# Kernel tuning notes

Measured on AMD Instinct MI355X. Metric: run time of the kernel, lower is better.

Reference implementation:

```python
import jax, jax.numpy as jnp
import numpy as np

N_NODES = 100000
N_EDGES = 800000
IN_SIZE = 256
OUT_SIZE = 256


def setup_inputs() -> dict:
    key = jax.random.key(0)
    k1, k2, k3, k4, k5, k6 = jax.random.split(key, 6)
    stdv = 1.0 / np.sqrt(OUT_SIZE)
    x = jax.random.normal(k1, (N_NODES, IN_SIZE), dtype=jnp.float32)
    weight = jax.random.uniform(k2, (IN_SIZE, OUT_SIZE), dtype=jnp.float32, minval=-stdv, maxval=stdv)
    bias = jax.random.uniform(k3, (1, OUT_SIZE), dtype=jnp.float32, minval=-stdv, maxval=stdv)
    edge_weight = jax.random.uniform(k4, (N_EDGES,), dtype=jnp.float32)
    edge_src = jax.random.randint(k5, (N_EDGES,), 0, N_NODES, dtype=jnp.int32)
    edge_dst = jax.random.randint(k6, (N_EDGES,), 0, N_NODES, dtype=jnp.int32)
    return {"x": x, "weight": weight, "bias": bias,
            "edge_weight": edge_weight, "edge_src": edge_src, "edge_dst": edge_dst}


def reference(x, weight, bias, edge_weight, edge_src, edge_dst):
    # supp = input @ W  (dense GEMM)
    supp = jnp.matmul(x, weight)  # [N, out]
    # out = spmm(A, supp): A in COO form -> gather source rows, scale, scatter-add to dst
    msgs = supp[edge_src] * edge_weight[:, None]  # [E, out]
    agg = jax.ops.segment_sum(msgs, edge_dst, num_segments=x.shape[0])  # [N, out]
    return agg + bias
```

## Files before the change

### kernel.cpp

```cpp
#include <hip/hip_runtime.h>
#include <hip/hip_bf16.h>

#define N_NODES 100000
#define N_EDGES 800000
#define K_DIM 256
#define N_DIM 256

typedef __attribute__((ext_vector_type(8)))  short  bf16x8;
typedef __attribute__((ext_vector_type(4)))  short  bf16x4;
typedef __attribute__((ext_vector_type(4)))  float  f32x4;

__device__ short g_Wt[K_DIM * N_DIM];
__device__ int   g_bsums[512];
__device__ int   g_boff[512];

static __device__ inline short f32_to_bf16s(float f) {
    __bf16 h = (__bf16)f;
    return __builtin_bit_cast(short, h);
}
static __device__ inline float bf16s_to_f32(short s) {
    unsigned int u = ((unsigned int)(unsigned short)s) << 16;
    return __uint_as_float(u);
}

__global__ __launch_bounds__(256) void convert_w_kernel(const float* __restrict__ W) {
    const int n = blockIdx.x;
    const int k = threadIdx.x;
    g_Wt[n * K_DIM + k] = f32_to_bf16s(W[(size_t)k * N_DIM + n]);
}

__global__ __launch_bounds__(256) void mfma_gemm_kernel(const float* __restrict__ X,
                                                        short* __restrict__ Sb,
                                                        int M) {
    const int wave = threadIdx.x >> 6;
    const int lane = threadIdx.x & 63;
    const int r    = lane & 15;
    const int kg   = lane >> 4;
    const int m0   = blockIdx.x * 64;
    const int wc   = wave * 64;

    f32x4 acc[4][4];
    #pragma unroll
    for (int i = 0; i < 4; ++i)
        #pragma unroll
        for (int j = 0; j < 4; ++j)
            acc[i][j] = (f32x4)0.f;

    #pragma unroll
    for (int k0 = 0; k0 < K_DIM; k0 += 32) {
        bf16x8 a[4], b[4];
        #pragma unroll
        for (int mi = 0; mi < 4; ++mi) {
            int row = m0 + mi * 16 + r;
            row = row < M ? row : (M - 1);
            const float* p = X + (size_t)row * K_DIM + k0 + kg * 8;
            f32x4 lo = *reinterpret_cast<const f32x4*>(p);
            f32x4 hi = *reinterpret_cast<const f32x4*>(p + 4);
            bf16x8 v;
            v[0] = f32_to_bf16s(lo[0]); v[1] = f32_to_bf16s(lo[1]);
            v[2] = f32_to_bf16s(lo[2]); v[3] = f32_to_bf16s(lo[3]);
            v[4] = f32_to_bf16s(hi[0]); v[5] = f32_to_bf16s(hi[1]);
            v[6] = f32_to_bf16s(hi[2]); v[7] = f32_to_bf16s(hi[3]);
            a[mi] = v;
        }
        #pragma unroll
        for (int ni = 0; ni < 4; ++ni) {
            const short* q = g_Wt + (size_t)(wc + ni * 16 + r) * K_DIM + k0 + kg * 8;
            b[ni] = *reinterpret_cast<const bf16x8*>(q);
        }
        #pragma unroll
        for (int mi = 0; mi < 4; ++mi)
            #pragma unroll
            for (int ni = 0; ni < 4; ++ni)
                acc[mi][ni] = __builtin_amdgcn_mfma_f32_16x16x32_bf16(a[mi], b[ni], acc[mi][ni], 0, 0, 0);
    }

    #pragma unroll
    for (int mi = 0; mi < 4; ++mi) {
        #pragma unroll
        for (int reg = 0; reg < 4; ++reg) {
            const int row = m0 + mi * 16 + kg * 4 + reg;
            if (row < M) {
                #pragma unroll
                for (int ni = 0; ni < 4; ++ni)
                    Sb[(size_t)row * N_DIM + wc + ni * 16 + r] = f32_to_bf16s(acc[mi][ni][reg]);
            }
        }
    }
}

__global__ __launch_bounds__(256) void count_kernel(const int* __restrict__ edst,
                                                    int* __restrict__ counts, int E) {
    int e = blockIdx.x * 256 + threadIdx.x;
    if (e < E) atomicAdd(&counts[edst[e]], 1);
}

#define SCAN_NB ((N_NODES + 255) / 256)

__global__ __launch_bounds__(256) void scan1_kernel(const int* __restrict__ counts) {
    __shared__ int wsum[4];
    const int i = blockIdx.x * 256 + threadIdx.x;
    int v = (i < N_NODES) ? counts[i] : 0;
    #pragma unroll
    for (int st = 32; st > 0; st >>= 1) v += __shfl_down(v, st, 64);
    if ((threadIdx.x & 63) == 0) wsum[threadIdx.x >> 6] = v;
    __syncthreads();
    if (threadIdx.x == 0) g_bsums[blockIdx.x] = wsum[0] + wsum[1] + wsum[2] + wsum[3];
}

__global__ __launch_bounds__(512) void scan2_kernel() {
    __shared__ int s[512];
    const int t = threadIdx.x;
    int v = (t < SCAN_NB) ? g_bsums[t] : 0;
    s[t] = v;
    __syncthreads();
    for (int st = 1; st < 512; st <<= 1) {
        int u = (t >= st) ? s[t - st] : 0;
        __syncthreads();
        s[t] += u;
        __syncthreads();
    }
    g_boff[t] = s[t] - v;
}

__global__ __launch_bounds__(256) void scan3_kernel(const int* __restrict__ counts,
                                                    int* __restrict__ offsets,
                                                    int* __restrict__ cursor) {
    __shared__ int s[256];
    const int t = threadIdx.x;
    const int i = blockIdx.x * 256 + t;
    int v = (i < N_NODES) ? counts[i] : 0;
    s[t] = v;
    __syncthreads();
    for (int st = 1; st < 256; st <<= 1) {
        int u = (t >= st) ? s[t - st] : 0;
        __syncthreads();
        s[t] += u;
        __syncthreads();
    }
    if (i < N_NODES) {
        int inc = g_boff[blockIdx.x] + s[t];
        offsets[i + 1] = inc;
        cursor[i]      = inc - v;
    }
    if (i == 0) offsets[0] = 0;
}

__global__ __launch_bounds__(256) void fill_kernel(const int* __restrict__ esrc,
                                                   const int* __restrict__ edst,
                                                   const float* __restrict__ ew,
                                                   int* __restrict__ cursor,
                                                   int2* __restrict__ csr, int E) {
    int e = blockIdx.x * 256 + threadIdx.x;
    if (e >= E) return;
    int pos = atomicAdd(&cursor[edst[e]], 1);
    csr[pos] = make_int2(esrc[e], __float_as_int(ew[e]));
}

__global__ __launch_bounds__(256) void gather_kernel(const short* __restrict__ Sb,
                                                     const float* __restrict__ bias,
                                                     const int* __restrict__ offsets,
                                                     const int2* __restrict__ csr,
                                                     float* __restrict__ out) {
    const int tid  = threadIdx.x;
    const int node = blockIdx.x * 4 + (tid >> 6);
    if (node >= N_NODES) return;
    const int lane = tid & 63;

    const int row = offsets[node];
    const int end = offsets[node + 1];

    f32x4 acc = *reinterpret_cast<const f32x4*>(bias + lane * 4);

    int j = row;
    for (; j + 2 <= end; j += 2) {
        const int2 p0 = csr[j];
        const int2 p1 = csr[j + 1];
        const bf16x4 v0 = *reinterpret_cast<const bf16x4*>(Sb + (size_t)p0.x * N_DIM + lane * 4);
        const bf16x4 v1 = *reinterpret_cast<const bf16x4*>(Sb + (size_t)p1.x * N_DIM + lane * 4);
        const float w0 = __int_as_float(p0.y);
        const float w1 = __int_as_float(p1.y);
        #pragma unroll
        for (int c = 0; c < 4; ++c)
            acc[c] += bf16s_to_f32(v0[c]) * w0 + bf16s_to_f32(v1[c]) * w1;
    }
    if (j < end) {
        const int2 p = csr[j];
        const bf16x4 v = *reinterpret_cast<const bf16x4*>(Sb + (size_t)p.x * N_DIM + lane * 4);
        const float w = __int_as_float(p.y);
        #pragma unroll
        for (int c = 0; c < 4; ++c)
            acc[c] += bf16s_to_f32(v[c]) * w;
    }

    *reinterpret_cast<f32x4*>(out + (size_t)node * N_DIM + lane * 4) = acc;
}

__global__ __launch_bounds__(256) void init_out_kernel(float* __restrict__ out,
                                                       const float* __restrict__ bias,
                                                       int total) {
    int i = blockIdx.x * 256 + threadIdx.x;
    if (i < total) out[i] = bias[i & (N_DIM - 1)];
}

__global__ __launch_bounds__(256) void scatter_kernel(const short* __restrict__ Sb,
                                                      const float* __restrict__ ew,
                                                      const int* __restrict__ esrc,
                                                      const int* __restrict__ edst,
                                                      float* __restrict__ out, int E) {
    const int tid  = threadIdx.x;
    const int e    = blockIdx.x * 4 + (tid >> 6);
    if (e >= E) return;
    const int lane = tid & 63;
    const int   s = esrc[e];
    const int   d = edst[e];
    const float w = ew[e];
    const bf16x4 v = *reinterpret_cast<const bf16x4*>(Sb + (size_t)s * N_DIM + lane * 4);
    float* o = out + (size_t)d * N_DIM + lane * 4;
    unsafeAtomicAdd(o + 0, bf16s_to_f32(v[0]) * w);
    unsafeAtomicAdd(o + 1, bf16s_to_f32(v[1]) * w);
    unsafeAtomicAdd(o + 2, bf16s_to_f32(v[2]) * w);
    unsafeAtomicAdd(o + 3, bf16s_to_f32(v[3]) * w);
}

extern "C" void kernel_launch(void* const* d_in, const int* in_sizes, int n_in,
                              void* d_out, int out_size, void* d_ws, size_t ws_size,
                              hipStream_t stream) {
    const float* x      = (const float*)d_in[0];
    const float* weight = (const float*)d_in[1];
    const float* bias   = (const float*)d_in[2];
    const float* ew     = (const float*)d_in[3];
    const int*   esrc   = (const int*)d_in[4];
    const int*   edst   = (const int*)d_in[5];
    float*       out    = (float*)d_out;

    char*  ws     = (char*)d_ws;
    const size_t SUPP_B = ((size_t)N_NODES * N_DIM * 2 + 255) & ~(size_t)255;
    const size_t CNT_B  = (size_t)N_NODES * 4;
    const size_t OFF_B  = ((size_t)(N_NODES + 1) * 4 + 15) & ~(size_t)15;
    const size_t CSR_B  = (size_t)N_EDGES * 8;

    short* supp    = (short*)(ws);
    int*   counts  = (int*)  (ws + SUPP_B);
    int*   cursor  = (int*)  (ws + SUPP_B + CNT_B);
    int*   offsets = (int*)  (ws + SUPP_B + 2 * CNT_B);
    int2*  csr     = (int2*) (ws + SUPP_B + 2 * CNT_B + OFF_B);
    const size_t NEEDED = SUPP_B + 2 * CNT_B + OFF_B + CSR_B;

    convert_w_kernel<<<N_DIM, 256, 0, stream>>>(weight);
    mfma_gemm_kernel<<<(N_NODES + 63) / 64, 256, 0, stream>>>(x, supp, N_NODES);

    if (ws_size >= NEEDED) {
        (void)hipMemsetAsync(counts, 0, CNT_B, stream);
        count_kernel<<<(N_EDGES + 255) / 256, 256, 0, stream>>>(edst, counts, N_EDGES);
        scan1_kernel<<<SCAN_NB, 256, 0, stream>>>(counts);
        scan2_kernel<<<1, 512, 0, stream>>>();
        scan3_kernel<<<SCAN_NB, 256, 0, stream>>>(counts, offsets, cursor);
        fill_kernel<<<(N_EDGES + 255) / 256, 256, 0, stream>>>(esrc, edst, ew,
                                                               cursor, csr, N_EDGES);
        gather_kernel<<<(N_NODES + 3) / 4, 256, 0, stream>>>(supp, bias, offsets, csr, out);
    } else {
        int total = N_NODES * N_DIM;
        init_out_kernel<<<(total + 255) / 256, 256, 0, stream>>>(out, bias, total);
        scatter_kernel<<<(N_EDGES + 3) / 4, 256, 0, stream>>>(supp, ew, esrc, edst, out, N_EDGES);
    }
}
```

Measured before the change: 414.1 us.

## Stage GEMM A tiles in LDS with double-buffered async global_load_lds

The fp32 X tile for each 64-row block is now loaded once per block into a double-buffered, XOR-swizzled LDS buffer using global_load_lds. Previously all four waves fetched the same A rows from global memory on their own. The load of the next K-slice overlaps with the current slice's MFMA work. The cost is extra LDS use and a barrier per K step, and correctness depends on the async LDS loads having completed before each barrier.

```diff
diff --git a/kernel.cpp b/kernel.cpp
--- a/kernel.cpp
+++ b/kernel.cpp
@@ -29,14 +29,20 @@
     g_Wt[n * K_DIM + k] = f32_to_bf16s(W[(size_t)k * N_DIM + n]);
 }
 
+#define GBM 64
+#define GBK 32
+
 __global__ __launch_bounds__(256) void mfma_gemm_kernel(const float* __restrict__ X,
                                                         short* __restrict__ Sb,
                                                         int M) {
-    const int wave = threadIdx.x >> 6;
-    const int lane = threadIdx.x & 63;
+    __shared__ float A_lds[2][GBM * GBK];
+
+    const int tid  = threadIdx.x;
+    const int wave = tid >> 6;
+    const int lane = tid & 63;
     const int r    = lane & 15;
     const int kg   = lane >> 4;
-    const int m0   = blockIdx.x * 64;
+    const int m0   = blockIdx.x * GBM;
     const int wc   = wave * 64;
 
     f32x4 acc[4][4];
@@ -46,16 +52,39 @@
         for (int j = 0; j < 4; ++j)
             acc[i][j] = (f32x4)0.f;
 
-    #pragma unroll
-    for (int k0 = 0; k0 < K_DIM; k0 += 32) {
-        bf16x8 a[4], b[4];
+    auto stage = [&](int buf, int k0) {
+        #pragma unroll
+        for (int p = 0; p < 2; ++p) {
+            const int d   = p * 256 + tid;
+            const int row = d >> 3;
+            const int cc  = (d & 7) ^ (row & 7);
+            int gr = m0 + row;
+            gr = gr < M ? gr : (M - 1);
+            const float* gp = X + (size_t)gr * K_DIM + k0 + cc * 4;
+            float* lp = &A_lds[buf][d * 4];
+            __builtin_amdgcn_global_load_lds(
+                (const __attribute__((address_space(1))) void*)gp,
+                (__attribute__((address_space(3))) void*)lp, 16, 0, 0);
+        }
+    };
+
+    stage(0, 0);
+    __syncthreads();
+
+    for (int t = 0; t < K_DIM / GBK; ++t) {
+        const int cur = t & 1;
+        if (t + 1 < K_DIM / GBK) stage(cur ^ 1, (t + 1) * GBK);
+
+        const int k0 = t * GBK;
+
+        bf16x8 a[4];
         #pragma unroll
         for (int mi = 0; mi < 4; ++mi) {
-            int row = m0 + mi * 16 + r;
-            row = row < M ? row : (M - 1);
-            const float* p = X + (size_t)row * K_DIM + k0 + kg * 8;
-            f32x4 lo = *reinterpret_cast<const f32x4*>(p);
-            f32x4 hi = *reinterpret_cast<const f32x4*>(p + 4);
+            const int rl = mi * 16 + r;
+            const int c0 = (kg * 2 + 0) ^ (rl & 7);
+            const int c1 = (kg * 2 + 1) ^ (rl & 7);
+            f32x4 lo = *reinterpret_cast<const f32x4*>(&A_lds[cur][rl * GBK + c0 * 4]);
+            f32x4 hi = *reinterpret_cast<const f32x4*>(&A_lds[cur][rl * GBK + c1 * 4]);
             bf16x8 v;
             v[0] = f32_to_bf16s(lo[0]); v[1] = f32_to_bf16s(lo[1]);
             v[2] = f32_to_bf16s(lo[2]); v[3] = f32_to_bf16s(lo[3]);
@@ -63,16 +92,21 @@
             v[6] = f32_to_bf16s(hi[2]); v[7] = f32_to_bf16s(hi[3]);
             a[mi] = v;
         }
+
+        bf16x8 b[4];
         #pragma unroll
         for (int ni = 0; ni < 4; ++ni) {
             const short* q = g_Wt + (size_t)(wc + ni * 16 + r) * K_DIM + k0 + kg * 8;
             b[ni] = *reinterpret_cast<const bf16x8*>(q);
         }
+
         #pragma unroll
         for (int mi = 0; mi < 4; ++mi)
             #pragma unroll
             for (int ni = 0; ni < 4; ++ni)
                 acc[mi][ni] = __builtin_amdgcn_mfma_f32_16x16x32_bf16(a[mi], b[ni], acc[mi][ni], 0, 0, 0);
+
+        __syncthreads();
     }
 
     #pragma unroll
@@ -248,7 +282,7 @@
     const size_t NEEDED = SUPP_B + 2 * CNT_B + OFF_B + CSR_B;
 
     convert_w_kernel<<<N_DIM, 256, 0, stream>>>(weight);
-    mfma_gemm_kernel<<<(N_NODES + 63) / 64, 256, 0, stream>>>(x, supp, N_NODES);
+    mfma_gemm_kernel<<<(N_NODES + GBM - 1) / GBM, 256, 0, stream>>>(x, supp, N_NODES);
 
     if (ws_size >= NEEDED) {
         (void)hipMemsetAsync(counts, 0, CNT_B, stream);
```

After: 377.5 us. -8.8%, faster.

## Stage X tile in swizzled LDS, fuse W convert with count, nontemporal gather

Applied to the files above, without the earlier changes.

The GEMM now loads and converts its 64x256 X tile to bf16 once into XOR-swizzled shared memory before the MFMA loop, instead of loading from global inside the k-loop. The W transpose/convert kernel is merged with the edge-count kernel into one launch, removing a launch. The gather kernel reads CSR entries and writes output with nontemporal loads and stores to cut cache pollution. The LDS tile costs 32KB per block, which may lower occupancy in exchange for coalesced global reads.

```diff
diff --git a/kernel.cpp b/kernel.cpp
--- a/kernel.cpp
+++ b/kernel.cpp
@@ -23,21 +23,55 @@
     return __uint_as_float(u);
 }
 
-__global__ __launch_bounds__(256) void convert_w_kernel(const float* __restrict__ W) {
-    const int n = blockIdx.x;
-    const int k = threadIdx.x;
-    g_Wt[n * K_DIM + k] = f32_to_bf16s(W[(size_t)k * N_DIM + n]);
-}
+__global__ __launch_bounds__(256) void convert_count_kernel(const float* __restrict__ W,
+                                                            const int* __restrict__ edst,
+                                                            int* __restrict__ counts,
+                                                            int E) {
+    const int b = blockIdx.x;
+    if (b < N_DIM) {
+        const int n = b;
+        const int k = threadIdx.x;
+        g_Wt[n * K_DIM + k] = f32_to_bf16s(W[(size_t)k * N_DIM + n]);
+    } else {
+        const int e = (b - N_DIM) * 256 + threadIdx.x;
+        if (e < E) atomicAdd(&counts[edst[e]], 1);
+    }
+}
+
+#define GBM 64
 
 __global__ __launch_bounds__(256) void mfma_gemm_kernel(const float* __restrict__ X,
                                                         short* __restrict__ Sb,
                                                         int M) {
-    const int wave = threadIdx.x >> 6;
-    const int lane = threadIdx.x & 63;
+    __shared__ short A_lds[GBM * K_DIM];
+
+    const int tid  = threadIdx.x;
+    const int wave = tid >> 6;
+    const int lane = tid & 63;
     const int r    = lane & 15;
     const int kg   = lane >> 4;
-    const int m0   = blockIdx.x * 64;
+    const int m0   = blockIdx.x * GBM;
     const int wc   = wave * 64;
+
+    #pragma unroll
+    for (int p = 0; p < 8; ++p) {
+        const int d   = p * 256 + tid;
+        const int row = d >> 5;
+        const int c   = d & 31;
+        const int cp  = (c & 24) | ((c ^ row) & 7);
+        int gr = m0 + row;
+        gr = gr < M ? gr : (M - 1);
+        const float* gp = X + (size_t)gr * K_DIM + c * 8;
+        f32x4 lo = *reinterpret_cast<const f32x4*>(gp);
+        f32x4 hi = *reinterpret_cast<const f32x4*>(gp + 4);
+        bf16x8 v;
+        v[0] = f32_to_bf16s(lo[0]); v[1] = f32_to_bf16s(lo[1]);
+        v[2] = f32_to_bf16s(lo[2]); v[3] = f32_to_bf16s(lo[3]);
+        v[4] = f32_to_bf16s(hi[0]); v[5] = f32_to_bf16s(hi[1]);
+        v[6] = f32_to_bf16s(hi[2]); v[7] = f32_to_bf16s(hi[3]);
+        *reinterpret_cast<bf16x8*>(&A_lds[row * K_DIM + cp * 8]) = v;
+    }
+    __syncthreads();
 
     f32x4 acc[4][4];
     #pragma unroll
@@ -47,21 +81,16 @@
             acc[i][j] = (f32x4)0.f;
 
     #pragma unroll
-    for (int k0 = 0; k0 < K_DIM; k0 += 32) {
+    for (int t = 0; t < K_DIM / 32; ++t) {
+        const int k0 = t * 32;
+
         bf16x8 a[4], b[4];
         #pragma unroll
         for (int mi = 0; mi < 4; ++mi) {
-            int row = m0 + mi * 16 + r;
-            row = row < M ? row : (M - 1);
-            const float* p = X + (size_t)row * K_DIM + k0 + kg * 8;
-            f32x4 lo = *reinterpret_cast<const f32x4*>(p);
-            f32x4 hi = *reinterpret_cast<const f32x4*>(p + 4);
-            bf16x8 v;
-            v[0] = f32_to_bf16s(lo[0]); v[1] = f32_to_bf16s(lo[1]);
-            v[2] = f32_to_bf16s(lo[2]); v[3] = f32_to_bf16s(lo[3]);
-            v[4] = f32_to_bf16s(hi[0]); v[5] = f32_to_bf16s(hi[1]);
-            v[6] = f32_to_bf16s(hi[2]); v[7] = f32_to_bf16s(hi[3]);
-            a[mi] = v;
+            const int rl = mi * 16 + r;
+            const int c  = 4 * t + kg;
+            const int cp = (c & 24) | ((c ^ rl) & 7);
+            a[mi] = *reinterpret_cast<const bf16x8*>(&A_lds[rl * K_DIM + cp * 8]);
         }
         #pragma unroll
         for (int ni = 0; ni < 4; ++ni) {
@@ -87,12 +116,6 @@
             }
         }
     }
-}
-
-__global__ __launch_bounds__(256) void count_kernel(const int* __restrict__ edst,
-                                                    int* __restrict__ counts, int E) {
-    int e = blockIdx.x * 256 + threadIdx.x;
-    if (e < E) atomicAdd(&counts[edst[e]], 1);
 }
 
 #define SCAN_NB ((N_NODES + 255) / 256)
@@ -160,7 +183,7 @@
 __global__ __launch_bounds__(256) void gather_kernel(const short* __restrict__ Sb,
                                                      const float* __restrict__ bias,
                                                      const int* __restrict__ offsets,
-                                                     const int2* __restrict__ csr,
+                                                     const long long* __restrict__ csr,
                                                      float* __restrict__ out) {
     const int tid  = threadIdx.x;
     const int node = blockIdx.x * 4 + (tid >> 6);
@@ -174,26 +197,29 @@
 
     int j = row;
     for (; j + 2 <= end; j += 2) {
-        const int2 p0 = csr[j];
-        const int2 p1 = csr[j + 1];
-        const bf16x4 v0 = *reinterpret_cast<const bf16x4*>(Sb + (size_t)p0.x * N_DIM + lane * 4);
-        const bf16x4 v1 = *reinterpret_cast<const bf16x4*>(Sb + (size_t)p1.x * N_DIM + lane * 4);
-        const float w0 = __int_as_float(p0.y);
-        const float w1 = __int_as_float(p1.y);
+        const long long q0 = __builtin_nontemporal_load(&csr[j]);
+        const long long q1 = __builtin_nontemporal_load(&csr[j + 1]);
+        const int   s0 = (int)(unsigned int)(q0 & 0xffffffffll);
+        const int   s1 = (int)(unsigned int)(q1 & 0xffffffffll);
+        const float w0 = __int_as_float((int)(q0 >> 32));
+        const float w1 = __int_as_float((int)(q1 >> 32));
+        const bf16x4 v0 = *reinterpret_cast<const bf16x4*>(Sb + (size_t)s0 * N_DIM + lane * 4);
+        const bf16x4 v1 = *reinterpret_cast<const bf16x4*>(Sb + (size_t)s1 * N_DIM + lane * 4);
         #pragma unroll
         for (int c = 0; c < 4; ++c)
             acc[c] += bf16s_to_f32(v0[c]) * w0 + bf16s_to_f32(v1[c]) * w1;
     }
     if (j < end) {
-        const int2 p = csr[j];
-        const bf16x4 v = *reinterpret_cast<const bf16x4*>(Sb + (size_t)p.x * N_DIM + lane * 4);
-        const float w = __int_as_float(p.y);
+        const long long q = __builtin_nontemporal_load(&csr[j]);
+        const int   s = (int)(unsigned int)(q & 0xffffffffll);
+        const float w = __int_as_float((int)(q >> 32));
+        const bf16x4 v = *reinterpret_cast<const bf16x4*>(Sb + (size_t)s * N_DIM + lane * 4);
         #pragma unroll
         for (int c = 0; c < 4; ++c)
             acc[c] += bf16s_to_f32(v[c]) * w;
     }
 
-    *reinterpret_cast<f32x4*>(out + (size_t)node * N_DIM + lane * 4) = acc;
+    __builtin_nontemporal_store(acc, reinterpret_cast<f32x4*>(out + (size_t)node * N_DIM + lane * 4));
 }
 
 __global__ __launch_bounds__(256) void init_out_kernel(float* __restrict__ out,
@@ -247,19 +273,21 @@
     int2*  csr     = (int2*) (ws + SUPP_B + 2 * CNT_B + OFF_B);
     const size_t NEEDED = SUPP_B + 2 * CNT_B + OFF_B + CSR_B;
 
-    convert_w_kernel<<<N_DIM, 256, 0, stream>>>(weight);
-    mfma_gemm_kernel<<<(N_NODES + 63) / 64, 256, 0, stream>>>(x, supp, N_NODES);
+    const int EDGE_NB = (N_EDGES + 255) / 256;
 
     if (ws_size >= NEEDED) {
         (void)hipMemsetAsync(counts, 0, CNT_B, stream);
-        count_kernel<<<(N_EDGES + 255) / 256, 256, 0, stream>>>(edst, counts, N_EDGES);
+        convert_count_kernel<<<N_DIM + EDGE_NB, 256, 0, stream>>>(weight, edst, counts, N_EDGES);
+        mfma_gemm_kernel<<<(N_NODES + GBM - 1) / GBM, 256, 0, stream>>>(x, supp, N_NODES);
         scan1_kernel<<<SCAN_NB, 256, 0, stream>>>(counts);
         scan2_kernel<<<1, 512, 0, stream>>>();
         scan3_kernel<<<SCAN_NB, 256, 0, stream>>>(counts, offsets, cursor);
-        fill_kernel<<<(N_EDGES + 255) / 256, 256, 0, stream>>>(esrc, edst, ew,
-                                                               cursor, csr, N_EDGES);
-        gather_kernel<<<(N_NODES + 3) / 4, 256, 0, stream>>>(supp, bias, offsets, csr, out);
+        fill_kernel<<<EDGE_NB, 256, 0, stream>>>(esrc, edst, ew, cursor, csr, N_EDGES);
+        gather_kernel<<<(N_NODES + 3) / 4, 256, 0, stream>>>(supp, bias, offsets,
+                                                             (const long long*)csr, out);
     } else {
+        convert_count_kernel<<<N_DIM, 256, 0, stream>>>(weight, edst,  (int*)d_ws, 0);
+        mfma_gemm_kernel<<<(N_NODES + GBM - 1) / GBM, 256, 0, stream>>>(x, supp, N_NODES);
         int total = N_NODES * N_DIM;
         init_out_kernel<<<(total + 255) / 256, 256, 0, stream>>>(out, bias, total);
         scatter_kernel<<<(N_EDGES + 3) / 4, 256, 0, stream>>>(supp, ew, esrc, edst, out, N_EDGES);
```

Measured after the change: 396.8 us. 1.04x faster.
